# Performance work log

Measured on AMD Instinct MI355X. Metric: run time of the kernel, lower is better.

## Reference

```python
import jax, jax.numpy as jnp
import numpy as np

DIM = 1024
ATT_DIM = 1024
NUM_HEADS = 16
HEAD_DIM = ATT_DIM // NUM_HEADS


def setup_inputs() -> dict:
    key = jax.random.key(0)
    ks = jax.random.split(key, 13)
    s = lambda fan_in: 1.0 / np.sqrt(fan_in)
    bsz, n = 8, 1024
    x = jax.random.normal(ks[0], (bsz, n, DIM), dtype=jnp.float32)
    # Linear weights stored as [in, out] (apply via x @ W + b)
    Wq = jax.random.uniform(ks[1], (DIM, ATT_DIM), minval=-s(DIM), maxval=s(DIM))
    bq = jax.random.uniform(ks[2], (ATT_DIM,), minval=-s(DIM), maxval=s(DIM))
    Wk = jax.random.uniform(ks[3], (DIM, ATT_DIM), minval=-s(DIM), maxval=s(DIM))
    bk = jax.random.uniform(ks[4], (ATT_DIM,), minval=-s(DIM), maxval=s(DIM))
    Wv = jax.random.uniform(ks[5], (DIM, ATT_DIM), minval=-s(DIM), maxval=s(DIM))
    bv = jax.random.uniform(ks[6], (ATT_DIM,), minval=-s(DIM), maxval=s(DIM))
    Win = jax.random.uniform(ks[7], (DIM, HEAD_DIM), minval=-s(DIM), maxval=s(DIM))
    bin_ = jax.random.uniform(ks[8], (HEAD_DIM,), minval=-s(DIM), maxval=s(DIM))
    d_in1 = HEAD_DIM * (NUM_HEADS + 1)
    W1 = jax.random.uniform(ks[9], (d_in1, 2 * DIM), minval=-s(d_in1), maxval=s(d_in1))
    b1 = jax.random.uniform(ks[10], (2 * DIM,), minval=-s(d_in1), maxval=s(d_in1))
    W2 = jax.random.uniform(ks[11], (2 * DIM, DIM), minval=-s(2 * DIM), maxval=s(2 * DIM))
    b2 = jax.random.uniform(ks[12], (DIM,), minval=-s(2 * DIM), maxval=s(2 * DIM))
    return {"x": x, "Wq": Wq, "bq": bq, "Wk": Wk, "bk": bk, "Wv": Wv, "bv": bv,
            "Win": Win, "bin_": bin_, "W1": W1, "b1": b1, "W2": W2, "b2": b2}


def reference(x, Wq, bq, Wk, bk, Wv, bv, Win, bin_, W1, b1, W2, b2):
    bsz, n, _ = x.shape
    scaling = HEAD_DIM ** (-0.5)
    # [b, n, h, d]
    q = (x @ Wq + bq).reshape(bsz, n, NUM_HEADS, HEAD_DIM) * scaling
    k = (x @ Wk + bk).reshape(bsz, n, NUM_HEADS, HEAD_DIM)
    v = (x @ Wv + bv).reshape(bsz, n, NUM_HEADS, HEAD_DIM)
    # scores [b, h, n, n]
    score = jnp.einsum('bihd,bjhd->bhij', q, k)
    diag = jnp.eye(n, dtype=bool)  # self positions masked with -inf
    score = jnp.where(diag[None, None], -jnp.inf, score)
    attn = jax.nn.softmax(score, axis=-1)
    out = jnp.einsum('bhij,bjhd->bihd', attn, v).reshape(bsz, n, NUM_HEADS * HEAD_DIM)
    in_ = (x @ Win + bin_)  # [b, n, head_dim]
    out = jnp.concatenate([out, in_], axis=-1)
    h = jax.nn.relu(out @ W1 + b1)
    return h @ W2 + b2
```

## Files before the change

### kernel.cpp

```cpp
#include <hip/hip_runtime.h>

typedef __bf16 bf16;
typedef __attribute__((ext_vector_type(8))) __bf16 bf16x8;
typedef __attribute__((ext_vector_type(4))) __bf16 bf16x4;
typedef __attribute__((ext_vector_type(4))) short short4_t;
typedef __attribute__((ext_vector_type(4))) float floatx4;

typedef const void __attribute__((address_space(1)))* gas1p;
typedef void __attribute__((address_space(3)))* las3p;

#define LOG2E 1.44269504088896340736f

static constexpr int D_MODEL = 1024;
static constexpr int N_HEADS = 16;
static constexpr int HDIM    = 64;
static constexpr int BSZ     = 8;
static constexpr int SEQ     = 1024;
static constexpr int ROWS    = BSZ * SEQ;
static constexpr int FF_IN   = 1088;
static constexpr int FF_HID  = 2048;
static constexpr int QKV_LD  = 3072;

__device__ __forceinline__ floatx4 mfma_bf16(bf16x8 a, bf16x8 b, floatx4 c) {
  return __builtin_amdgcn_mfma_f32_16x16x32_bf16(a, b, c, 0, 0, 0);
}

__device__ __forceinline__ floatx4 mfma16(bf16x4 a, bf16x4 b, floatx4 c) {
#if __has_builtin(__builtin_amdgcn_mfma_f32_16x16x16_bf16)
  return __builtin_amdgcn_mfma_f32_16x16x16_bf16(a, b, c, 0, 0, 0);
#else
  return __builtin_amdgcn_mfma_f32_16x16x16bf16_1k(
      __builtin_bit_cast(short4_t, a), __builtin_bit_cast(short4_t, b), c, 0, 0, 0);
#endif
}

__device__ __forceinline__ float flex_load(const void* src, size_t idx, int isbf) {
  return isbf ? (float)((const bf16*)src)[idx] : ((const float*)src)[idx];
}

__global__ void detect_kernel(const unsigned* __restrict__ w, int* __restrict__ flag) {
  __shared__ int cnt;
  if (threadIdx.x == 0) cnt = 0;
  __syncthreads();
  int hits = 0;
  for (int i = threadIdx.x; i < 4096; i += 256) {
    const unsigned v = w[(size_t)i * 997 + 13];
    const unsigned b = (v >> 8) & 0x7F;
    hits += (b >= 0x3B && b <= 0x41) ? 1 : 0;
  }
  atomicAdd(&cnt, hits);
  __syncthreads();
  if (threadIdx.x == 0) *flag = (cnt > 2048) ? 1 : 0;
}

__global__ __launch_bounds__(256)
void x_to_bf16_kernel(const void* __restrict__ src, bf16* __restrict__ dst,
                      const int* __restrict__ flag) {
  const int isbf = *flag;
  const size_t i = ((size_t)blockIdx.x * 256 + threadIdx.x) * 4;
  bf16x4 o;
  if (isbf) {
    o = *reinterpret_cast<const bf16x4*>((const bf16*)src + i);
  } else {
    const float4 f = *reinterpret_cast<const float4*>((const float*)src + i);
    o[0] = (bf16)f.x; o[1] = (bf16)f.y; o[2] = (bf16)f.z; o[3] = (bf16)f.w;
  }
  *reinterpret_cast<bf16x4*>(dst + i) = o;
}

__global__ __launch_bounds__(256)
void bias_all_kernel(const void* bq, const void* bk, const void* bv,
                     const void* bin, const void* b1, const void* b2,
                     float* __restrict__ dst, const int* __restrict__ flag) {
  const int isbf = *flag;
  const int i = blockIdx.x * 256 + threadIdx.x;
  if (i < 1024)      dst[i] = flex_load(bq, i, isbf) * 0.125f;
  else if (i < 2048) dst[i] = flex_load(bk, i - 1024, isbf);
  else if (i < 3072) dst[i] = flex_load(bv, i - 2048, isbf);
  else if (i < 3136) dst[i] = flex_load(bin, i - 3072, isbf);
  else if (i < 5184) dst[i] = flex_load(b1, i - 3136, isbf);
  else if (i < 6208) dst[i] = flex_load(b2, i - 5184, isbf);
}

struct TransJobs {
  const void* src[6];
  bf16* dst[6];
  int R[6], C[6];
  int tiles_x[6];
  int tile_base[7];
  float scale[6];
};

__global__ __launch_bounds__(256)
void transpose_all_kernel(TransJobs J, const int* __restrict__ flag) {
  __shared__ float tile[32][33];
  const int isbf = *flag;
  const int bid = blockIdx.x;
  int j = 0;
#pragma unroll
  for (int t = 1; t < 6; t++) j += (bid >= J.tile_base[t]) ? 1 : 0;
  const int t = bid - J.tile_base[j];
  const int c0 = (t % J.tiles_x[j]) * 32, r0 = (t / J.tiles_x[j]) * 32;
  const void* src = J.src[j];
  bf16* dst = J.dst[j];
  const int R = J.R[j], C = J.C[j];
  const float scale = J.scale[j];
  const int tx = threadIdx.x & 31, ty = threadIdx.x >> 5;
  for (int i = ty; i < 32; i += 8)
    tile[i][tx] = flex_load(src, (size_t)(r0 + i) * C + (c0 + tx), isbf);
  __syncthreads();
  for (int i = ty; i < 32; i += 8)
    dst[(size_t)(c0 + i) * R + (r0 + tx)] = (bf16)(tile[tx][i] * scale);
}

__global__ __launch_bounds__(256)
void transpose_v_kernel(const bf16* __restrict__ v, bf16* __restrict__ vt) {
  __shared__ float tile[32][33];
  const int bh = blockIdx.z, b = bh >> 4, h = bh & 15;
  const int s0 = blockIdx.x * 32, d0 = blockIdx.y * 32;
  const int tx = threadIdx.x & 31, ty = threadIdx.x >> 5;
  const bf16* src = v + (size_t)b * SEQ * QKV_LD + 2048 + h * HDIM;
  bf16* dst = vt + (size_t)bh * HDIM * SEQ;
  for (int i = ty; i < 32; i += 8)
    tile[i][tx] = (float)src[(size_t)(s0 + i) * QKV_LD + d0 + tx];
  __syncthreads();
  for (int i = ty; i < 32; i += 8)
    dst[(size_t)(d0 + i) * SEQ + s0 + tx] = (bf16)tile[tx][i];
}

template <int BN, bool DO_RELU, bool OUT_FLEX>
__global__ __launch_bounds__(256)
void gemm_bt(const bf16* __restrict__ A, const bf16* __restrict__ BT,
             const float* __restrict__ bias,
             void* __restrict__ Cv, int M, int N, int K, int ldc,
             const int* __restrict__ flag) {
  constexpr int BM = 128, BK = 32;
  constexpr int TCN = BN / 32;
  constexpr int ACH = (BM * BK) / (256 * 8);
  constexpr int BCH = (BN * BK) / (256 * 8);
  __shared__ bf16 As[BM * BK];
  __shared__ bf16 Bs[BN * BK];
  const int tid = threadIdx.x;
  const int wave = tid >> 6, lane = tid & 63;
  const int quad = lane >> 4, lo = lane & 15;
  const int wm = wave >> 1, wn = wave & 1;
  const int m0 = blockIdx.x * BM;
  const int n0 = blockIdx.y * BN;

  floatx4 acc[4][TCN];
#pragma unroll
  for (int i = 0; i < 4; i++)
#pragma unroll
    for (int j = 0; j < TCN; j++) acc[i][j] = floatx4{0.f, 0.f, 0.f, 0.f};

  for (int kb = 0; kb < K; kb += BK) {
#pragma unroll
    for (int u = 0; u < ACH; u++) {
      const int c = u * 256 + tid;
      const int row = c >> 2, cc = c & 3;
      const bf16* g = A + (size_t)(m0 + row) * K + kb + cc * 8;
      __builtin_amdgcn_global_load_lds((gas1p)g, (las3p)(As + c * 8), 16, 0, 0);
    }
#pragma unroll
    for (int u = 0; u < BCH; u++) {
      const int c = u * 256 + tid;
      const int row = c >> 2, cc = c & 3;
      const bf16* g = BT + (size_t)(n0 + row) * K + kb + cc * 8;
      __builtin_amdgcn_global_load_lds((gas1p)g, (las3p)(Bs + c * 8), 16, 0, 0);
    }
    __syncthreads();
    bf16x8 af[4], bfr[TCN];
#pragma unroll
    for (int tr = 0; tr < 4; tr++)
      af[tr] = *reinterpret_cast<const bf16x8*>(As + (wm * 64 + tr * 16 + lo) * BK + quad * 8);
#pragma unroll
    for (int tc = 0; tc < TCN; tc++)
      bfr[tc] = *reinterpret_cast<const bf16x8*>(Bs + (wn * (BN / 2) + tc * 16 + lo) * BK + quad * 8);
#pragma unroll
    for (int tr = 0; tr < 4; tr++)
#pragma unroll
      for (int tc = 0; tc < TCN; tc++)
        acc[tr][tc] = mfma_bf16(af[tr], bfr[tc], acc[tr][tc]);
    __syncthreads();
  }

  const int isbf = OUT_FLEX ? *flag : 1;
#pragma unroll
  for (int tc = 0; tc < TCN; tc++) {
    const int col = n0 + wn * (BN / 2) + tc * 16 + lo;
    const float bval = bias[col];
#pragma unroll
    for (int tr = 0; tr < 4; tr++) {
      const int rbase = m0 + wm * 64 + tr * 16 + quad * 4;
#pragma unroll
      for (int r = 0; r < 4; r++) {
        float v = acc[tr][tc][r] + bval;
        if (DO_RELU) v = fmaxf(v, 0.f);
        const size_t idx = (size_t)(rbase + r) * ldc + col;
        if (!OUT_FLEX || isbf) ((bf16*)Cv)[idx] = (bf16)v;
        else                   ((float*)Cv)[idx] = v;
      }
    }
  }
}

__global__ __launch_bounds__(256)
void attn_kernel(const bf16* __restrict__ QKV, const bf16* __restrict__ Vt,
                 bf16* __restrict__ Cc) {
  __shared__ bf16 Ks[64 * 64];
  __shared__ bf16 Vs[64 * 64];
  const int bid = blockIdx.x;
  const int xcd = bid & 7, g = bid >> 3;
  const int ib = g & 7, bh = (g >> 3) * 8 + xcd;
  const int b = bh >> 4, h = bh & 15;
  const int i0 = ib * 128;
  const int tid = threadIdx.x, wave = tid >> 6, lane = tid & 63;
  const int quad = lane >> 4, lo = lane & 15;
  const int iw = i0 + wave * 32;
  const bf16* qptr = QKV + (size_t)b * SEQ * QKV_LD + h * HDIM;
  const bf16* kptr = QKV + (size_t)b * SEQ * QKV_LD + 1024 + h * HDIM;
  const bf16* vptr = Vt + (size_t)bh * HDIM * SEQ;

  bf16x8 qf[2][2];
#pragma unroll
  for (int it = 0; it < 2; it++)
#pragma unroll
    for (int kf = 0; kf < 2; kf++)
      qf[it][kf] = *reinterpret_cast<const bf16x8*>(
          qptr + (size_t)(iw + it * 16 + lo) * QKV_LD + kf * 32 + quad * 8);

  floatx4 oacc[2][4];
  float lrow[2] = {0.f, 0.f};
#pragma unroll
  for (int it = 0; it < 2; it++)
#pragma unroll
    for (int dt = 0; dt < 4; dt++) oacc[it][dt] = floatx4{0.f, 0.f, 0.f, 0.f};

  for (int jb = 0; jb < SEQ / 64; jb++) {
    const int j0 = jb * 64;
#pragma unroll
    for (int u = 0; u < 2; u++) {
      const int c = u * 256 + tid;
      const int row = c >> 3, col = c & 7;
      const int gcol = col ^ (row & 7);
      __builtin_amdgcn_global_load_lds(
          (gas1p)(kptr + (size_t)(j0 + row) * QKV_LD + gcol * 8),
          (las3p)(Ks + c * 8), 16, 0, 0);
      __builtin_amdgcn_global_load_lds(
          (gas1p)(vptr + (size_t)row * SEQ + j0 + gcol * 8),
          (las3p)(Vs + c * 8), 16, 0, 0);
    }
    __syncthreads();

    floatx4 sacc[2][4];
#pragma unroll
    for (int it = 0; it < 2; it++)
#pragma unroll
      for (int mt = 0; mt < 4; mt++) sacc[it][mt] = floatx4{0.f, 0.f, 0.f, 0.f};
#pragma unroll
    for (int mt = 0; mt < 4; mt++) {
      const int r = mt * 16 + lo;
      const int cc0 = quad ^ (lo & 7);
      const int cc1 = (4 + quad) ^ (lo & 7);
      const bf16x8 k0 = *reinterpret_cast<const bf16x8*>(Ks + r * 64 + cc0 * 8);
      const bf16x8 k1 = *reinterpret_cast<const bf16x8*>(Ks + r * 64 + cc1 * 8);
#pragma unroll
      for (int it = 0; it < 2; it++) {
        sacc[it][mt] = mfma_bf16(k0, qf[it][0], sacc[it][mt]);
        sacc[it][mt] = mfma_bf16(k1, qf[it][1], sacc[it][mt]);
      }
    }

    if (j0 == (iw & ~63)) {
#pragma unroll
      for (int it = 0; it < 2; it++) {
        const int ig = iw + it * 16 + lo;
#pragma unroll
        for (int mt = 0; mt < 4; mt++)
#pragma unroll
          for (int r = 0; r < 4; r++)
            if (j0 + mt * 16 + quad * 4 + r == ig) sacc[it][mt][r] = -1e30f;
      }
    }

    bf16x4 pfrag[2][4];
#pragma unroll
    for (int it = 0; it < 2; it++) {
      float s = 0.f;
#pragma unroll
      for (int mt = 0; mt < 4; mt++) {
        bf16x4 pk;
#pragma unroll
        for (int r = 0; r < 4; r++) {
          const float p = exp2f(sacc[it][mt][r] * LOG2E);
          s += p;
          pk[r] = (bf16)p;
        }
        pfrag[it][mt] = pk;
      }
      s += __shfl_xor(s, 16);
      s += __shfl_xor(s, 32);
      lrow[it] += s;
    }

#pragma unroll
    for (int dt = 0; dt < 4; dt++) {
      const int r = dt * 16 + lo;
#pragma unroll
      for (int kt = 0; kt < 4; kt++) {
        const int gch = kt * 2 + (quad >> 1);
        const int cc = gch ^ (lo & 7);
        const bf16x4 vf = *reinterpret_cast<const bf16x4*>(
            Vs + r * 64 + cc * 8 + (quad & 1) * 4);
#pragma unroll
        for (int it = 0; it < 2; it++)
          oacc[it][dt] = mfma16(vf, pfrag[it][kt], oacc[it][dt]);
      }
    }
    __syncthreads();
  }

#pragma unroll
  for (int it = 0; it < 2; it++) {
    const int ig = iw + it * 16 + lo;
    const float inv = 1.0f / lrow[it];
    bf16* cb = Cc + ((size_t)b * SEQ + ig) * FF_IN + h * HDIM;
#pragma unroll
    for (int dt = 0; dt < 4; dt++) {
      bf16x4 o;
#pragma unroll
      for (int r = 0; r < 4; r++) o[r] = (bf16)(oacc[it][dt][r] * inv);
      *reinterpret_cast<bf16x4*>(cb + dt * 16 + quad * 4) = o;
    }
  }
}

extern "C" void kernel_launch(void* const* d_in, const int* in_sizes, int n_in,
                              void* d_out, int out_size, void* d_ws, size_t ws_size,
                              hipStream_t stream) {
  (void)in_sizes; (void)n_in; (void)out_size; (void)ws_size;
  const void* x   = d_in[0];
  const void* Wq  = d_in[1];
  const void* bq  = d_in[2];
  const void* Wk  = d_in[3];
  const void* bk  = d_in[4];
  const void* Wv  = d_in[5];
  const void* bv  = d_in[6];
  const void* Win = d_in[7];
  const void* bin = d_in[8];
  const void* W1  = d_in[9];
  const void* b1  = d_in[10];
  const void* W2  = d_in[11];
  const void* b2  = d_in[12];

  size_t off = 0;
  char* wsb = (char*)d_ws;
  auto alloc = [&](size_t bytes) {
    void* p = (void*)(wsb + off);
    off += (bytes + 255) & ~(size_t)255;
    return p;
  };
  int*   flag  = (int*)alloc(4);
  bf16*  xbf   = (bf16*)alloc((size_t)ROWS * D_MODEL * 2);
  bf16*  WqkvT = (bf16*)alloc((size_t)QKV_LD * 1024 * 2);
  bf16*  WinT  = (bf16*)alloc((size_t)64 * 1024 * 2);
  bf16*  W1T   = (bf16*)alloc((size_t)FF_HID * FF_IN * 2);
  bf16*  W2T   = (bf16*)alloc((size_t)D_MODEL * FF_HID * 2);
  float* biasf = (float*)alloc(6208 * 4);
  bf16*  qkv   = (bf16*)alloc((size_t)ROWS * QKV_LD * 2);
  bf16*  vtb   = (bf16*)alloc((size_t)ROWS * D_MODEL * 2);
  bf16*  cbuf  = (bf16*)alloc((size_t)ROWS * FF_IN * 2);
  bf16*  hbuf  = (bf16*)alloc((size_t)ROWS * FF_HID * 2);
  float* bqkvf = biasf;
  float* binf  = biasf + 3072;
  float* b1f   = biasf + 3136;
  float* b2f   = biasf + 5184;

  const dim3 blk(256);
  detect_kernel<<<1, blk, 0, stream>>>((const unsigned*)x, flag);

  x_to_bf16_kernel<<<(ROWS * D_MODEL) / 1024, blk, 0, stream>>>(x, xbf, flag);
  bias_all_kernel<<<25, blk, 0, stream>>>(bq, bk, bv, bin, b1, b2, biasf, flag);

  TransJobs J;
  J.src[0] = Wq;  J.dst[0] = WqkvT;                        J.R[0] = 1024; J.C[0] = 1024; J.scale[0] = 0.125f;
  J.src[1] = Wk;  J.dst[1] = WqkvT + (size_t)1024 * 1024;  J.R[1] = 1024; J.C[1] = 1024; J.scale[1] = 1.0f;
  J.src[2] = Wv;  J.dst[2] = WqkvT + (size_t)2048 * 1024;  J.R[2] = 1024; J.C[2] = 1024; J.scale[2] = 1.0f;
  J.src[3] = Win; J.dst[3] = WinT;                         J.R[3] = 1024; J.C[3] = 64;   J.scale[3] = 1.0f;
  J.src[4] = W1;  J.dst[4] = W1T;                          J.R[4] = 1088; J.C[4] = 2048; J.scale[4] = 1.0f;
  J.src[5] = W2;  J.dst[5] = W2T;                          J.R[5] = 2048; J.C[5] = 1024; J.scale[5] = 1.0f;
  int base = 0;
  for (int j = 0; j < 6; j++) {
    J.tiles_x[j] = J.C[j] / 32;
    J.tile_base[j] = base;
    base += (J.R[j] / 32) * (J.C[j] / 32);
  }
  J.tile_base[6] = base;
  transpose_all_kernel<<<base, blk, 0, stream>>>(J, flag);

  gemm_bt<128, false, false><<<dim3(ROWS / 128, QKV_LD / 128), blk, 0, stream>>>(
      xbf, WqkvT, bqkvf, qkv, ROWS, QKV_LD, 1024, QKV_LD, nullptr);
  gemm_bt<64, false, false><<<dim3(ROWS / 128, 1), blk, 0, stream>>>(
      xbf, WinT, binf, cbuf + 1024, ROWS, 64, 1024, FF_IN, nullptr);

  transpose_v_kernel<<<dim3(SEQ / 32, HDIM / 32, BSZ * N_HEADS), blk, 0, stream>>>(qkv, vtb);

  attn_kernel<<<dim3(1024), blk, 0, stream>>>(qkv, vtb, cbuf);

  gemm_bt<128, true, false><<<dim3(ROWS / 128, FF_HID / 128), blk, 0, stream>>>(
      cbuf, W1T, b1f, hbuf, ROWS, FF_HID, FF_IN, FF_HID, nullptr);
  gemm_bt<128, false, true><<<dim3(ROWS / 128, D_MODEL / 128), blk, 0, stream>>>(
      hbuf, W2T, b2f, d_out, ROWS, D_MODEL, FF_HID, D_MODEL, flag);
}
```

Before: 446.1 us.

## Double GEMM K-tile with XOR-swizzled LDS, fuse Win projection into QKV GEMM

Raises the GEMM K-tile from 32 to 64 and XOR-swizzles the 16-byte chunk placement in LDS, so each block issues half as many barrier/load rounds and the MFMA fragment reads avoid bank conflicts. The Win projection is appended as extra columns of the QKV weight matrix and handled by the same GEMM launch, with a split epilogue that writes those columns into the concat buffer. The x conversion kernel now handles 8 elements per thread. The fused launch also computes 64 padding columns whose weights come from uninitialised workspace, and the larger tile doubles LDS use per block.

```diff
diff --git a/kernel.cpp b/kernel.cpp
--- a/kernel.cpp
+++ b/kernel.cpp
@@ -57,15 +57,17 @@
 void x_to_bf16_kernel(const void* __restrict__ src, bf16* __restrict__ dst,
                       const int* __restrict__ flag) {
   const int isbf = *flag;
-  const size_t i = ((size_t)blockIdx.x * 256 + threadIdx.x) * 4;
-  bf16x4 o;
+  const size_t i = ((size_t)blockIdx.x * 256 + threadIdx.x) * 8;
+  bf16x8 o;
   if (isbf) {
-    o = *reinterpret_cast<const bf16x4*>((const bf16*)src + i);
+    o = *reinterpret_cast<const bf16x8*>((const bf16*)src + i);
   } else {
-    const float4 f = *reinterpret_cast<const float4*>((const float*)src + i);
-    o[0] = (bf16)f.x; o[1] = (bf16)f.y; o[2] = (bf16)f.z; o[3] = (bf16)f.w;
-  }
-  *reinterpret_cast<bf16x4*>(dst + i) = o;
+    const float4 f0 = *reinterpret_cast<const float4*>((const float*)src + i);
+    const float4 f1 = *reinterpret_cast<const float4*>((const float*)src + i + 4);
+    o[0] = (bf16)f0.x; o[1] = (bf16)f0.y; o[2] = (bf16)f0.z; o[3] = (bf16)f0.w;
+    o[4] = (bf16)f1.x; o[5] = (bf16)f1.y; o[6] = (bf16)f1.z; o[7] = (bf16)f1.w;
+  }
+  *reinterpret_cast<bf16x8*>(dst + i) = o;
 }
 
 __global__ __launch_bounds__(256)
@@ -132,9 +134,10 @@
 __global__ __launch_bounds__(256)
 void gemm_bt(const bf16* __restrict__ A, const bf16* __restrict__ BT,
              const float* __restrict__ bias,
-             void* __restrict__ Cv, int M, int N, int K, int ldc,
+             void* __restrict__ Cv, int N, int K, int ldc,
+             bf16* __restrict__ C2, int ldc2, int nsplit, int nvalid,
              const int* __restrict__ flag) {
-  constexpr int BM = 128, BK = 32;
+  constexpr int BM = 128, BK = 64;
   constexpr int TCN = BN / 32;
   constexpr int ACH = (BM * BK) / (256 * 8);
   constexpr int BCH = (BN * BK) / (256 * 8);
@@ -157,30 +160,41 @@
 #pragma unroll
     for (int u = 0; u < ACH; u++) {
       const int c = u * 256 + tid;
-      const int row = c >> 2, cc = c & 3;
-      const bf16* g = A + (size_t)(m0 + row) * K + kb + cc * 8;
+      const int row = c >> 3, col = c & 7;
+      const int gcol = col ^ (row & 7);
+      const bf16* g = A + (size_t)(m0 + row) * K + kb + gcol * 8;
       __builtin_amdgcn_global_load_lds((gas1p)g, (las3p)(As + c * 8), 16, 0, 0);
     }
 #pragma unroll
     for (int u = 0; u < BCH; u++) {
       const int c = u * 256 + tid;
-      const int row = c >> 2, cc = c & 3;
-      const bf16* g = BT + (size_t)(n0 + row) * K + kb + cc * 8;
+      const int row = c >> 3, col = c & 7;
+      const int gcol = col ^ (row & 7);
+      const bf16* g = BT + (size_t)(n0 + row) * K + kb + gcol * 8;
       __builtin_amdgcn_global_load_lds((gas1p)g, (las3p)(Bs + c * 8), 16, 0, 0);
     }
     __syncthreads();
-    bf16x8 af[4], bfr[TCN];
-#pragma unroll
-    for (int tr = 0; tr < 4; tr++)
-      af[tr] = *reinterpret_cast<const bf16x8*>(As + (wm * 64 + tr * 16 + lo) * BK + quad * 8);
-#pragma unroll
-    for (int tc = 0; tc < TCN; tc++)
-      bfr[tc] = *reinterpret_cast<const bf16x8*>(Bs + (wn * (BN / 2) + tc * 16 + lo) * BK + quad * 8);
-#pragma unroll
-    for (int tr = 0; tr < 4; tr++)
-#pragma unroll
-      for (int tc = 0; tc < TCN; tc++)
-        acc[tr][tc] = mfma_bf16(af[tr], bfr[tc], acc[tr][tc]);
+#pragma unroll
+    for (int kk = 0; kk < 2; kk++) {
+      bf16x8 af[4], bfr[TCN];
+#pragma unroll
+      for (int tr = 0; tr < 4; tr++) {
+        const int row = wm * 64 + tr * 16 + lo;
+        const int cc = (kk * 4 + quad) ^ (lo & 7);
+        af[tr] = *reinterpret_cast<const bf16x8*>(As + row * BK + cc * 8);
+      }
+#pragma unroll
+      for (int tc = 0; tc < TCN; tc++) {
+        const int row = wn * (BN / 2) + tc * 16 + lo;
+        const int cc = (kk * 4 + quad) ^ (lo & 7);
+        bfr[tc] = *reinterpret_cast<const bf16x8*>(Bs + row * BK + cc * 8);
+      }
+#pragma unroll
+      for (int tr = 0; tr < 4; tr++)
+#pragma unroll
+        for (int tc = 0; tc < TCN; tc++)
+          acc[tr][tc] = mfma_bf16(af[tr], bfr[tc], acc[tr][tc]);
+    }
     __syncthreads();
   }
 
@@ -189,16 +203,29 @@
   for (int tc = 0; tc < TCN; tc++) {
     const int col = n0 + wn * (BN / 2) + tc * 16 + lo;
     const float bval = bias[col];
-#pragma unroll
-    for (int tr = 0; tr < 4; tr++) {
-      const int rbase = m0 + wm * 64 + tr * 16 + quad * 4;
-#pragma unroll
-      for (int r = 0; r < 4; r++) {
-        float v = acc[tr][tc][r] + bval;
-        if (DO_RELU) v = fmaxf(v, 0.f);
-        const size_t idx = (size_t)(rbase + r) * ldc + col;
-        if (!OUT_FLEX || isbf) ((bf16*)Cv)[idx] = (bf16)v;
-        else                   ((float*)Cv)[idx] = v;
+    if (col < nsplit) {
+#pragma unroll
+      for (int tr = 0; tr < 4; tr++) {
+        const int rbase = m0 + wm * 64 + tr * 16 + quad * 4;
+#pragma unroll
+        for (int r = 0; r < 4; r++) {
+          float v = acc[tr][tc][r] + bval;
+          if (DO_RELU) v = fmaxf(v, 0.f);
+          const size_t idx = (size_t)(rbase + r) * ldc + col;
+          if (!OUT_FLEX || isbf) ((bf16*)Cv)[idx] = (bf16)v;
+          else                   ((float*)Cv)[idx] = v;
+        }
+      }
+    } else if (col < nvalid) {
+#pragma unroll
+      for (int tr = 0; tr < 4; tr++) {
+        const int rbase = m0 + wm * 64 + tr * 16 + quad * 4;
+#pragma unroll
+        for (int r = 0; r < 4; r++) {
+          float v = acc[tr][tc][r] + bval;
+          if (DO_RELU) v = fmaxf(v, 0.f);
+          C2[(size_t)(rbase + r) * ldc2 + (col - nsplit)] = (bf16)v;
+        }
       }
     }
   }
@@ -362,8 +389,7 @@
   };
   int*   flag  = (int*)alloc(4);
   bf16*  xbf   = (bf16*)alloc((size_t)ROWS * D_MODEL * 2);
-  bf16*  WqkvT = (bf16*)alloc((size_t)QKV_LD * 1024 * 2);
-  bf16*  WinT  = (bf16*)alloc((size_t)64 * 1024 * 2);
+  bf16*  WqkvT = (bf16*)alloc((size_t)3200 * 1024 * 2);
   bf16*  W1T   = (bf16*)alloc((size_t)FF_HID * FF_IN * 2);
   bf16*  W2T   = (bf16*)alloc((size_t)D_MODEL * FF_HID * 2);
   float* biasf = (float*)alloc(6208 * 4);
@@ -371,22 +397,20 @@
   bf16*  vtb   = (bf16*)alloc((size_t)ROWS * D_MODEL * 2);
   bf16*  cbuf  = (bf16*)alloc((size_t)ROWS * FF_IN * 2);
   bf16*  hbuf  = (bf16*)alloc((size_t)ROWS * FF_HID * 2);
-  float* bqkvf = biasf;
-  float* binf  = biasf + 3072;
   float* b1f   = biasf + 3136;
   float* b2f   = biasf + 5184;
 
   const dim3 blk(256);
   detect_kernel<<<1, blk, 0, stream>>>((const unsigned*)x, flag);
 
-  x_to_bf16_kernel<<<(ROWS * D_MODEL) / 1024, blk, 0, stream>>>(x, xbf, flag);
+  x_to_bf16_kernel<<<(ROWS * D_MODEL) / 2048, blk, 0, stream>>>(x, xbf, flag);
   bias_all_kernel<<<25, blk, 0, stream>>>(bq, bk, bv, bin, b1, b2, biasf, flag);
 
   TransJobs J;
   J.src[0] = Wq;  J.dst[0] = WqkvT;                        J.R[0] = 1024; J.C[0] = 1024; J.scale[0] = 0.125f;
   J.src[1] = Wk;  J.dst[1] = WqkvT + (size_t)1024 * 1024;  J.R[1] = 1024; J.C[1] = 1024; J.scale[1] = 1.0f;
   J.src[2] = Wv;  J.dst[2] = WqkvT + (size_t)2048 * 1024;  J.R[2] = 1024; J.C[2] = 1024; J.scale[2] = 1.0f;
-  J.src[3] = Win; J.dst[3] = WinT;                         J.R[3] = 1024; J.C[3] = 64;   J.scale[3] = 1.0f;
+  J.src[3] = Win; J.dst[3] = WqkvT + (size_t)3072 * 1024;  J.R[3] = 1024; J.C[3] = 64;   J.scale[3] = 1.0f;
   J.src[4] = W1;  J.dst[4] = W1T;                          J.R[4] = 1088; J.C[4] = 2048; J.scale[4] = 1.0f;
   J.src[5] = W2;  J.dst[5] = W2T;                          J.R[5] = 2048; J.C[5] = 1024; J.scale[5] = 1.0f;
   int base = 0;
@@ -398,17 +422,18 @@
   J.tile_base[6] = base;
   transpose_all_kernel<<<base, blk, 0, stream>>>(J, flag);
 
-  gemm_bt<128, false, false><<<dim3(ROWS / 128, QKV_LD / 128), blk, 0, stream>>>(
-      xbf, WqkvT, bqkvf, qkv, ROWS, QKV_LD, 1024, QKV_LD, nullptr);
-  gemm_bt<64, false, false><<<dim3(ROWS / 128, 1), blk, 0, stream>>>(
-      xbf, WinT, binf, cbuf + 1024, ROWS, 64, 1024, FF_IN, nullptr);
+  gemm_bt<128, false, false><<<dim3(ROWS / 128, 25), blk, 0, stream>>>(
+      xbf, WqkvT, biasf, qkv, 3200, 1024, QKV_LD,
+      cbuf + 1024, FF_IN, 3072, 3136, nullptr);
 
   transpose_v_kernel<<<dim3(SEQ / 32, HDIM / 32, BSZ * N_HEADS), blk, 0, stream>>>(qkv, vtb);
 
   attn_kernel<<<dim3(1024), blk, 0, stream>>>(qkv, vtb, cbuf);
 
   gemm_bt<128, true, false><<<dim3(ROWS / 128, FF_HID / 128), blk, 0, stream>>>(
-      cbuf, W1T, b1f, hbuf, ROWS, FF_HID, FF_IN, FF_HID, nullptr);
+      cbuf, W1T, b1f, hbuf, FF_HID, FF_IN, FF_HID,
+      nullptr, 0, FF_HID, FF_HID, nullptr);
   gemm_bt<128, false, true><<<dim3(ROWS / 128, D_MODEL / 128), blk, 0, stream>>>(
-      hbuf, W2T, b2f, d_out, ROWS, D_MODEL, FF_HID, D_MODEL, flag);
-}
+      hbuf, W2T, b2f, d_out, D_MODEL, FF_HID, D_MODEL,
+      nullptr, 0, D_MODEL, D_MODEL, flag);
+}
```

Result: faster. 411.4 us (-7.8%).
